# Kernel optimization log

Measured on AMD Instinct MI355X. Metric: run time of the kernel, lower is better.

Reference implementation:

```python
import jax, jax.numpy as jnp
import numpy as np

NEG_INF = -1e38


def wkv(k, v, w, u):
    """Log-sum-exp-stabilized RWKV WKV scan.
    k, v: (B, T, C); w, u: (C,). Returns y: (B, T, C).
    """
    B, T, C = k.shape

    def step(carry, kv_t):
        num, den, mx = carry            # each (B, C)
        k_t, v_t = kv_t                 # (B, C)
        ku = k_t + u
        m = jnp.maximum(mx, ku)
        e1 = jnp.exp(mx - m)
        e2 = jnp.exp(ku - m)
        y = (e1 * num + e2 * v_t) / (e1 * den + e2)
        # state update
        mw = mx + w
        m2 = jnp.maximum(mw, k_t)
        es1 = jnp.exp(mw - m2)
        es2 = jnp.exp(k_t - m2)
        num = es1 * num + es2 * v_t
        den = es1 * den + es2
        return (num, den, m2), y

    init = (jnp.zeros((B, C), k.dtype),
            jnp.zeros((B, C), k.dtype),
            jnp.full((B, C), NEG_INF, k.dtype))
    _, y = jax.lax.scan(step, init, (jnp.swapaxes(k, 0, 1), jnp.swapaxes(v, 0, 1)))
    return jnp.swapaxes(y, 0, 1)


def setup_inputs() -> dict:
    key = jax.random.key(0)
    ks = jax.random.split(key, 8)
    B, T, C = 8, 4096, 512
    x = jax.random.normal(ks[0], (B, T, C), dtype=jnp.float32)
    # Linear weights stored as (in, out) so forward is x @ W.
    W_rkv = jax.random.normal(ks[1], (C, 6 * C), dtype=jnp.float32) / np.sqrt(C)
    W_out = jax.random.normal(ks[2], (2 * C, C), dtype=jnp.float32) / np.sqrt(2 * C)
    time_decay = jax.random.uniform(ks[3], (C,), minval=-6.0, maxval=-5.0, dtype=jnp.float32)
    time_first = jax.random.uniform(ks[4], (C,), minval=-3.0, maxval=0.0, dtype=jnp.float32)
    time_decay_rev = jax.random.uniform(ks[5], (C,), minval=-6.0, maxval=-5.0, dtype=jnp.float32)
    time_first_rev = jax.random.uniform(ks[6], (C,), minval=-3.0, maxval=0.0, dtype=jnp.float32)
    return {"x": x, "W_rkv": W_rkv, "W_out": W_out,
            "time_decay": time_decay, "time_first": time_first,
            "time_decay_rev": time_decay_rev, "time_first_rev": time_first_rev}


def reference(x, W_rkv, W_out, time_decay, time_first, time_decay_rev, time_first_rev):
    B, T, C = x.shape
    rkv = (x @ W_rkv).reshape(B, T, 2, 3, C)
    # forward direction
    r_f, k_f, v_f = rkv[:, :, 0, 0], rkv[:, :, 0, 1], rkv[:, :, 0, 2]
    w_f = -jnp.exp(time_decay)
    out_f = jax.nn.sigmoid(r_f) * wkv(k_f, v_f, w_f, time_first)
    # backward direction (run scan on time-reversed k/v, then reverse back)
    r_b, k_b, v_b = rkv[:, :, 1, 0], rkv[:, :, 1, 1], rkv[:, :, 1, 2]
    w_b = -jnp.exp(time_decay_rev)
    out_b = wkv(k_b[:, ::-1], v_b[:, ::-1], w_b, time_first_rev)[:, ::-1]
    out_b = jax.nn.sigmoid(r_b) * out_b
    out_cat = jnp.concatenate([out_f, out_b], axis=-1)  # (B, T, 2C)
    return out_cat @ W_out
```

## Files before the change

### kernel.cpp

```cpp
#include <hip/hip_runtime.h>

typedef float f4 __attribute__((ext_vector_type(4)));
typedef unsigned short us4 __attribute__((ext_vector_type(4)));
typedef __bf16 bf16x8 __attribute__((ext_vector_type(8)));
typedef float f32x4 __attribute__((ext_vector_type(4)));
typedef _Float16 h4 __attribute__((ext_vector_type(4)));
typedef _Float16 h8 __attribute__((ext_vector_type(8)));

#define TT 4096
#define CCH 512
#define NCH2 256
#define CHL2 16
#define NSEG 32
#define SEGC 8

__device__ __forceinline__ unsigned short f2bf(float f) {
  unsigned u = __builtin_bit_cast(unsigned, f);
  unsigned r = (u + 0x7FFFu + ((u >> 16) & 1u)) >> 16;
  return (unsigned short)r;
}
__device__ __forceinline__ void gload_lds16(const void* g, void* l) {
  __builtin_amdgcn_global_load_lds(
      (const __attribute__((address_space(1))) unsigned int*)g,
      (__attribute__((address_space(3))) unsigned int*)l, 16, 0, 0);
}
#define VMCNT(n) asm volatile("s_waitcnt vmcnt(" #n ")" ::: "memory")

__global__ __launch_bounds__(256)
void convert_f32_bf16(const float* __restrict__ in, unsigned short* __restrict__ out, int n4) {
  int i = blockIdx.x * 256 + threadIdx.x;
  if (i >= n4) return;
  f4 f = *(const f4*)(in + (size_t)i * 4);
  us4 o = { f2bf(f[0]), f2bf(f[1]), f2bf(f[2]), f2bf(f[3]) };
  *(us4*)(out + (size_t)i * 4) = o;
}

__global__ __launch_bounds__(256)
void transpose_to_bf16(const float* __restrict__ in, unsigned short* __restrict__ out,
                       int R, int Cc) {
  __shared__ unsigned short tile[32][33];
  int c0 = blockIdx.x * 32, r0 = blockIdx.y * 32;
  int tx = threadIdx.x, ty = threadIdx.y;
  #pragma unroll
  for (int j = 0; j < 32; j += 8)
    tile[ty + j][tx] = f2bf(in[(size_t)(r0 + ty + j) * Cc + c0 + tx]);
  __syncthreads();
  #pragma unroll
  for (int j = 0; j < 32; j += 8)
    out[(size_t)(c0 + ty + j) * R + r0 + tx] = tile[tx][ty + j];
}

__global__ __launch_bounds__(512, 2)
void gemm256_g1(const unsigned short* __restrict__ A,
                const unsigned short* __restrict__ BT,
                _Float16* __restrict__ kbuf, _Float16* __restrict__ vbuf,
                _Float16* __restrict__ rbuf) {
  __shared__ char lds[131072];
  const int tid = threadIdx.x;
  const int lane = tid & 63, wv = tid >> 6;
  const int wm = wv >> 2, wn = wv & 3;
  const int ln15 = lane & 15, lq = lane >> 4;

  const int nwg = gridDim.x;
  const int bid = blockIdx.x;
  const int wgid = (nwg % 8 == 0) ? (bid % 8) * (nwg / 8) + bid / 8 : bid;
  const int bn = wgid % 12, bm = wgid / 12;
  const size_t m0 = (size_t)bm * 256, n0 = (size_t)bn * 256;
  const char* Ab = (const char*)(A + m0 * 512);
  const char* Bb = (const char*)(BT + n0 * 512);

  const int srow0 = tid >> 2, srow1 = 128 + (tid >> 2);
  const int sg = tid & 3;
  const int sgs0 = (sg ^ ((srow0 >> 1) & 3)) << 4;
  const int sgs1 = (sg ^ ((srow1 >> 1) & 3)) << 4;

  auto STAGE = [&](int mat, int t, int h) {
    const char* gsrc = mat ? Bb : Ab;
    char* ldst = lds + mat * 65536 + ((t & 1) << 15) + (h << 14);
    const size_t co = (size_t)t * 128 + (size_t)h * 64;
    gload_lds16(gsrc + (size_t)srow0 * 1024 + co + sgs0, ldst + tid * 16);
    gload_lds16(gsrc + (size_t)srow1 * 1024 + co + sgs1, ldst + 8192 + tid * 16);
  };

  f32x4 acc[8][4] = {};
  STAGE(0, 0, 0); STAGE(1, 0, 0); STAGE(0, 0, 1); STAGE(1, 0, 1);

  for (int t = 0; t < 8; ++t) {
    char* Abase = lds + ((t & 1) << 15);
    char* Bbase = lds + 65536 + ((t & 1) << 15);
    VMCNT(4);
    __builtin_amdgcn_s_barrier();
    __builtin_amdgcn_sched_barrier(0);
    {
      bf16x8 bf[4], af[8];
      #pragma unroll
      for (int fn = 0; fn < 4; ++fn) {
        const int r = wn * 64 + fn * 16 + ln15;
        bf[fn] = *(const bf16x8*)(Bbase + r * 64 + ((lq ^ ((r >> 1) & 3)) << 4));
      }
      #pragma unroll
      for (int fm = 0; fm < 8; ++fm) {
        const int r = wm * 128 + fm * 16 + ln15;
        af[fm] = *(const bf16x8*)(Abase + r * 64 + ((lq ^ ((r >> 1) & 3)) << 4));
      }
      if (t < 7) { STAGE(0, t + 1, 0); STAGE(1, t + 1, 0); }
      __builtin_amdgcn_s_setprio(1);
      #pragma unroll
      for (int fm = 0; fm < 8; ++fm)
        #pragma unroll
        for (int fn = 0; fn < 4; ++fn)
          acc[fm][fn] = __builtin_amdgcn_mfma_f32_16x16x32_bf16(af[fm], bf[fn], acc[fm][fn], 0, 0, 0);
      __builtin_amdgcn_s_setprio(0);
    }
    if (t < 7) { VMCNT(4); } else { VMCNT(0); }
    __builtin_amdgcn_s_barrier();
    __builtin_amdgcn_sched_barrier(0);
    {
      bf16x8 bf[4], af[8];
      #pragma unroll
      for (int fn = 0; fn < 4; ++fn) {
        const int r = wn * 64 + fn * 16 + ln15;
        bf[fn] = *(const bf16x8*)(Bbase + 16384 + r * 64 + ((lq ^ ((r >> 1) & 3)) << 4));
      }
      #pragma unroll
      for (int fm = 0; fm < 8; ++fm) {
        const int r = wm * 128 + fm * 16 + ln15;
        af[fm] = *(const bf16x8*)(Abase + 16384 + r * 64 + ((lq ^ ((r >> 1) & 3)) << 4));
      }
      if (t < 7) { STAGE(0, t + 1, 1); STAGE(1, t + 1, 1); }
      __builtin_amdgcn_s_setprio(1);
      #pragma unroll
      for (int fm = 0; fm < 8; ++fm)
        #pragma unroll
        for (int fn = 0; fn < 4; ++fn)
          acc[fm][fn] = __builtin_amdgcn_mfma_f32_16x16x32_bf16(af[fm], bf[fn], acc[fm][fn], 0, 0, 0);
      __builtin_amdgcn_s_setprio(0);
    }
  }

  const int n0i = (int)n0;
  const int dir = (n0i >= 1536) ? 1 : 0;
  const int jj0 = n0i - dir * 1536;
  const int seg = jj0 >> 9;
  const int cbase = jj0 & 511;
  _Float16* dbuf = (seg == 0) ? rbuf : (seg == 1 ? kbuf : vbuf);
  float* stg = (float*)lds;
  const int ebnd = wv >> 2;
  const int erow = (tid >> 3) & 31;
  const int el8 = tid & 7;
  __syncthreads();
  #pragma unroll
  for (int gi = 0; gi < 4; ++gi) {
    #pragma unroll
    for (int f2 = 0; f2 < 2; ++f2) {
      const int fm = gi * 2 + f2;
      #pragma unroll
      for (int q = 0; q < 4; ++q) {
        const int rloc = f2 * 16 + lq * 4 + q;
        float* dst = stg + wm * 8192 + rloc * 256;
        const int sw = ((rloc >> 2) & 1) << 4;
        #pragma unroll
        for (int fn = 0; fn < 4; ++fn)
          dst[(wn * 64 + fn * 16 + ln15) ^ sw] = acc[fm][fn][q];
      }
    }
    __syncthreads();
    {
      const int rowg = (int)m0 + ebnd * 128 + gi * 32 + erow;
      const int b_ = rowg >> 12, tt = rowg & 4095;
      const int trow = dir ? (4095 - tt) : tt;
      _Float16* gp = dbuf + ((size_t)(b_ * 2 + dir) * TT + trow) * 512 + cbase;
      const float* sp = stg + ebnd * 8192 + erow * 256;
      const int sw = ((erow >> 2) & 1) << 4;
      #pragma unroll
      for (int u = 0; u < 4; ++u) {
        const int cf = el8 * 8 + u * 64;
        const int cs = cf ^ sw;
        f4 a = *(const f4*)(sp + cs);
        f4 b = *(const f4*)(sp + cs + 4);
        h8 hv = { (_Float16)a[0], (_Float16)a[1], (_Float16)a[2], (_Float16)a[3],
                  (_Float16)b[0], (_Float16)b[1], (_Float16)b[2], (_Float16)b[3] };
        *(h8*)(gp + cf) = hv;
      }
    }
    __syncthreads();
  }
}

__global__ __launch_bounds__(256)
void gemm_bf16_m1(const unsigned short* __restrict__ A, int lda,
                  const unsigned short* __restrict__ BT, int ldb,
                  int M, int N, int K, float* __restrict__ out) {
  __shared__ char smem[16384];
  unsigned short* As  = (unsigned short*)smem;
  unsigned short* Bsm = (unsigned short*)(smem + 8192);
  const int tid = threadIdx.x;
  const int lane = tid & 63, wv = tid >> 6;
  const int wr = wv >> 1, wc = wv & 1;
  const int ln15 = lane & 15, lq = lane >> 4;
  const int mtiles = M >> 7;
  const int bm = blockIdx.x % mtiles, bn = blockIdx.x / mtiles;
  const size_t m0 = (size_t)bm << 7, n0 = (size_t)bn << 7;
  f32x4 acc[4][4] = {};
  const char* Ab = (const char*)(A + m0 * (size_t)lda);
  const char* Bb = (const char*)(BT + n0 * (size_t)ldb);
  const int r0 = tid >> 2;
  const int cb = (((tid & 3) ^ (r0 & 3)) << 4);
  const size_t ldab = (size_t)lda * 2, ldbb = (size_t)ldb * 2;

  for (int k0 = 0; k0 < K; k0 += 32) {
    const size_t kb = (size_t)k0 * 2;
    gload_lds16(Ab + (size_t)r0 * ldab + kb + cb,        (char*)As + tid * 16);
    gload_lds16(Ab + (size_t)(r0 + 64) * ldab + kb + cb, (char*)As + 4096 + tid * 16);
    gload_lds16(Bb + (size_t)r0 * ldbb + kb + cb,        (char*)Bsm + tid * 16);
    gload_lds16(Bb + (size_t)(r0 + 64) * ldbb + kb + cb, (char*)Bsm + 4096 + tid * 16);
    __syncthreads();
    bf16x8 af[4], bg[4];
    #pragma unroll
    for (int i = 0; i < 4; ++i) {
      const int ar = wr * 64 + i * 16 + ln15;
      const int br = wc * 64 + i * 16 + ln15;
      af[i] = *(const bf16x8*)((char*)As  + ((ar * 4 + (lq ^ (ar & 3))) << 4));
      bg[i] = *(const bf16x8*)((char*)Bsm + ((br * 4 + (lq ^ (br & 3))) << 4));
    }
    #pragma unroll
    for (int i = 0; i < 4; ++i)
      #pragma unroll
      for (int j = 0; j < 4; ++j)
        acc[i][j] = __builtin_amdgcn_mfma_f32_16x16x32_bf16(af[i], bg[j], acc[i][j], 0, 0, 0);
    __syncthreads();
  }

  const int tq = tid >> 3, t8 = tid & 7;
  #pragma unroll
  for (int i = 0; i < 4; ++i) {
    __syncthreads();
    float* st = (float*)smem;
    #pragma unroll
    for (int j = 0; j < 4; ++j) {
      const int cl = wc * 64 + j * 16 + ln15;
      #pragma unroll
      for (int q = 0; q < 4; ++q) {
        const int rl = wr * 16 + lq * 4 + q;
        st[rl * 128 + (cl ^ (((rl >> 2) & 3) << 4))] = acc[i][j][q];
      }
    }
    __syncthreads();
    const int rl = tq, lqp = (rl >> 2) & 3;
    const int lr = ((rl >> 4) << 6) + (i << 4) + (rl & 15);
    const int rowg = (int)m0 + lr;
    #pragma unroll
    for (int u = 0; u < 4; ++u) {
      const int colL = t8 * 16 + u * 4;
      const int colS = colL ^ (lqp << 4);
      f4 vv = *(const f4*)(st + rl * 128 + colS);
      *(f4*)(out + (size_t)rowg * N + n0 + colL) = vv;
    }
  }
}

__global__ __launch_bounds__(128)
void wkv_pass1(const _Float16* __restrict__ kbuf, const _Float16* __restrict__ vbuf,
               const float* __restrict__ td, const float* __restrict__ tdr,
               float* __restrict__ cN, float* __restrict__ cD, float* __restrict__ cM) {
  const int bd = blockIdx.x;
  const int ch = blockIdx.y;
  const int dir = bd & 1;
  const int c = threadIdx.x * 4;
  f4 tdv = *(const f4*)((dir ? tdr : td) + c);
  float w[4], num[4], den[4], m[4];
  #pragma unroll
  for (int e = 0; e < 4; ++e) { w[e] = -__expf(tdv[e]); num[e] = 0.f; den[e] = 0.f; m[e] = -1e38f; }
  const size_t base = ((size_t)bd * TT + (size_t)ch * CHL2) * CCH + c;
  const _Float16* kp = kbuf + base;
  const _Float16* vp = vbuf + base;
  h4 ka = *(const h4*)(kp), va = *(const h4*)(vp);
  h4 kb = *(const h4*)(kp + CCH), vb = *(const h4*)(vp + CCH);
  for (int t = 0; t < CHL2; ++t) {
    h4 kc = {}, vc = {};
    if (t + 2 < CHL2) {
      kc = *(const h4*)(kp + (size_t)(t + 2) * CCH);
      vc = *(const h4*)(vp + (size_t)(t + 2) * CCH);
    }
    #pragma unroll
    for (int e = 0; e < 4; ++e) {
      float ke = (float)ka[e], ve = (float)va[e];
      float mw = m[e] + w[e];
      float m2 = fmaxf(mw, ke);
      float e1 = __expf(mw - m2), e2 = __expf(ke - m2);
      num[e] = e1 * num[e] + e2 * ve;
      den[e] = e1 * den[e] + e2;
      m[e] = m2;
    }
    ka = kb; va = vb; kb = kc; vb = vc;
  }
  const size_t ci = ((size_t)bd * NCH2 + ch) * CCH + c;
  *(f4*)(cN + ci) = (f4){num[0], num[1], num[2], num[3]};
  *(f4*)(cD + ci) = (f4){den[0], den[1], den[2], den[3]};
  *(f4*)(cM + ci) = (f4){m[0], m[1], m[2], m[3]};
}

__global__ __launch_bounds__(128)
void wkv_p2a(const float* __restrict__ td, const float* __restrict__ tdr,
             const float* __restrict__ cN, const float* __restrict__ cD,
             const float* __restrict__ cM,
             float* __restrict__ scN, float* __restrict__ scD, float* __restrict__ scM) {
  const int bd = blockIdx.x, seg = blockIdx.y;
  const int dir = bd & 1;
  const int c = threadIdx.x * 4;
  f4 tdv = *(const f4*)((dir ? tdr : td) + c);
  float dw[4], num[4], den[4], m[4];
  #pragma unroll
  for (int e = 0; e < 4; ++e) { dw[e] = -__expf(tdv[e]) * (float)CHL2; num[e] = 0.f; den[e] = 0.f; m[e] = -1e38f; }
  size_t ci = ((size_t)bd * NCH2 + (size_t)seg * SEGC) * CCH + c;
  for (int j = 0; j < SEGC; ++j, ci += CCH) {
    f4 ln = *(const f4*)(cN + ci);
    f4 ld = *(const f4*)(cD + ci);
    f4 lm = *(const f4*)(cM + ci);
    #pragma unroll
    for (int e = 0; e < 4; ++e) {
      float mp = m[e] + dw[e];
      float mm = fmaxf(mp, lm[e]);
      float e1 = __expf(mp - mm), e2 = __expf(lm[e] - mm);
      num[e] = e1 * num[e] + e2 * ln[e];
      den[e] = e1 * den[e] + e2 * ld[e];
      m[e] = mm;
    }
  }
  const size_t si = ((size_t)bd * NSEG + seg) * CCH + c;
  *(f4*)(scN + si) = (f4){num[0], num[1], num[2], num[3]};
  *(f4*)(scD + si) = (f4){den[0], den[1], den[2], den[3]};
  *(f4*)(scM + si) = (f4){m[0], m[1], m[2], m[3]};
}

__global__ __launch_bounds__(128)
void wkv_p2b(const float* __restrict__ td, const float* __restrict__ tdr,
             float* __restrict__ scN, float* __restrict__ scD, float* __restrict__ scM) {
  const int bd = blockIdx.x;
  const int dir = bd & 1;
  const int c = threadIdx.x * 4;
  f4 tdv = *(const f4*)((dir ? tdr : td) + c);
  float dws[4], num[4], den[4], m[4];
  #pragma unroll
  for (int e = 0; e < 4; ++e) { dws[e] = -__expf(tdv[e]) * (float)(CHL2 * SEGC); num[e] = 0.f; den[e] = 0.f; m[e] = -1e38f; }
  size_t si = (size_t)bd * NSEG * CCH + c;
  for (int s = 0; s < NSEG; ++s, si += CCH) {
    f4 ln = *(const f4*)(scN + si);
    f4 ld = *(const f4*)(scD + si);
    f4 lm = *(const f4*)(scM + si);
    *(f4*)(scN + si) = (f4){num[0], num[1], num[2], num[3]};
    *(f4*)(scD + si) = (f4){den[0], den[1], den[2], den[3]};
    *(f4*)(scM + si) = (f4){m[0], m[1], m[2], m[3]};
    #pragma unroll
    for (int e = 0; e < 4; ++e) {
      float mp = m[e] + dws[e];
      float mm = fmaxf(mp, lm[e]);
      float e1 = __expf(mp - mm), e2 = __expf(lm[e] - mm);
      num[e] = e1 * num[e] + e2 * ln[e];
      den[e] = e1 * den[e] + e2 * ld[e];
      m[e] = mm;
    }
  }
}

__global__ __launch_bounds__(128)
void wkv_p2c(const float* __restrict__ td, const float* __restrict__ tdr,
             const float* __restrict__ scN, const float* __restrict__ scD,
             const float* __restrict__ scM,
             float* __restrict__ cN, float* __restrict__ cD, float* __restrict__ cM) {
  const int bd = blockIdx.x, seg = blockIdx.y;
  const int dir = bd & 1;
  const int c = threadIdx.x * 4;
  f4 tdv = *(const f4*)((dir ? tdr : td) + c);
  const size_t si = ((size_t)bd * NSEG + seg) * CCH + c;
  f4 nv = *(const f4*)(scN + si);
  f4 dv = *(const f4*)(scD + si);
  f4 mv = *(const f4*)(scM + si);
  float dw[4], num[4], den[4], m[4];
  #pragma unroll
  for (int e = 0; e < 4; ++e) {
    dw[e] = -__expf(tdv[e]) * (float)CHL2;
    num[e] = nv[e]; den[e] = dv[e]; m[e] = mv[e];
  }
  size_t ci = ((size_t)bd * NCH2 + (size_t)seg * SEGC) * CCH + c;
  for (int j = 0; j < SEGC; ++j, ci += CCH) {
    f4 ln = *(const f4*)(cN + ci);
    f4 ld = *(const f4*)(cD + ci);
    f4 lm = *(const f4*)(cM + ci);
    *(f4*)(cN + ci) = (f4){num[0], num[1], num[2], num[3]};
    *(f4*)(cD + ci) = (f4){den[0], den[1], den[2], den[3]};
    *(f4*)(cM + ci) = (f4){m[0], m[1], m[2], m[3]};
    #pragma unroll
    for (int e = 0; e < 4; ++e) {
      float mp = m[e] + dw[e];
      float mm = fmaxf(mp, lm[e]);
      float e1 = __expf(mp - mm), e2 = __expf(lm[e] - mm);
      num[e] = e1 * num[e] + e2 * ln[e];
      den[e] = e1 * den[e] + e2 * ld[e];
      m[e] = mm;
    }
  }
}

__global__ __launch_bounds__(128)
void wkv_pass3(const _Float16* __restrict__ kbuf, const _Float16* __restrict__ vbuf,
               const _Float16* __restrict__ rbuf,
               const float* __restrict__ td, const float* __restrict__ tf,
               const float* __restrict__ tdr, const float* __restrict__ tfr,
               const float* __restrict__ cN, const float* __restrict__ cD,
               const float* __restrict__ cM,
               unsigned short* __restrict__ ocat) {
  const int bd = blockIdx.x, ch = blockIdx.y;
  const int b = bd >> 1, dir = bd & 1;
  const int c = threadIdx.x * 4;
  f4 tdv = *(const f4*)((dir ? tdr : td) + c);
  f4 tuv = *(const f4*)((dir ? tfr : tf) + c);
  const size_t ci = ((size_t)bd * NCH2 + ch) * CCH + c;
  f4 nv = *(const f4*)(cN + ci);
  f4 dv = *(const f4*)(cD + ci);
  f4 mv = *(const f4*)(cM + ci);
  float w[4], u[4], num[4], den[4], m[4];
  #pragma unroll
  for (int e = 0; e < 4; ++e) {
    w[e] = -__expf(tdv[e]); u[e] = tuv[e];
    num[e] = nv[e]; den[e] = dv[e]; m[e] = mv[e];
  }
  const size_t base = ((size_t)bd * TT + (size_t)ch * CHL2) * CCH + c;
  const _Float16* kp = kbuf + base;
  const _Float16* vp = vbuf + base;
  const _Float16* rp = rbuf + base;
  h4 ka = *(const h4*)(kp), va = *(const h4*)(vp), ra = *(const h4*)(rp);
  h4 kb = *(const h4*)(kp + CCH), vb = *(const h4*)(vp + CCH), rb = *(const h4*)(rp + CCH);
  for (int t = 0; t < CHL2; ++t) {
    h4 kc = {}, vc = {}, rc = {};
    if (t + 2 < CHL2) {
      kc = *(const h4*)(kp + (size_t)(t + 2) * CCH);
      vc = *(const h4*)(vp + (size_t)(t + 2) * CCH);
      rc = *(const h4*)(rp + (size_t)(t + 2) * CCH);
    }
    const int tnat = ch * CHL2 + t;
    const int tact = dir ? (TT - 1 - tnat) : tnat;
    unsigned short o[4];
    #pragma unroll
    for (int e = 0; e < 4; ++e) {
      float ke = (float)ka[e], ve = (float)va[e];
      float ku = ke + u[e];
      float mm = fmaxf(m[e], ku);
      float e1 = __expf(m[e] - mm), e2 = __expf(ku - mm);
      float y = (e1 * num[e] + e2 * ve) * __builtin_amdgcn_rcpf(e1 * den[e] + e2);
      float rt = (float)ra[e];
      float sig = __builtin_amdgcn_rcpf(1.f + __expf(-rt));
      o[e] = f2bf(sig * y);
      float mw = m[e] + w[e];
      float m2 = fmaxf(mw, ke);
      float es1 = __expf(mw - m2), es2 = __expf(ke - m2);
      num[e] = es1 * num[e] + es2 * ve;
      den[e] = es1 * den[e] + es2;
      m[e] = m2;
    }
    *(us4*)(ocat + (((size_t)b * TT + tact) * 2 + dir) * CCH + c) = (us4){o[0], o[1], o[2], o[3]};
    ka = kb; va = vb; ra = rb; kb = kc; vb = vc; rb = rc;
  }
}

extern "C" void kernel_launch(void* const* d_in, const int* in_sizes, int n_in,
                              void* d_out, int out_size, void* d_ws, size_t ws_size,
                              hipStream_t stream) {
  const float* x   = (const float*)d_in[0];
  const float* Wr  = (const float*)d_in[1];
  const float* Wo  = (const float*)d_in[2];
  const float* td  = (const float*)d_in[3];
  const float* tf  = (const float*)d_in[4];
  const float* tdr = (const float*)d_in[5];
  const float* tfr = (const float*)d_in[6];
  float* out = (float*)d_out;

  auto rnd = [](size_t b) { return (b + 255) & ~(size_t)255; };
  const size_t wBytes = rnd((size_t)3072 * 512 * 2) + rnd((size_t)512 * 1024 * 2);
  auto need = [&](int Bs) {
    size_t s = wBytes;
    s += 3 * rnd((size_t)Bs * 2 * TT * 512 * 2);
    s += rnd((size_t)Bs * TT * 1024 * 2);
    s += 3 * rnd((size_t)Bs * 2 * (size_t)NCH2 * 512 * 4);
    s += 3 * rnd((size_t)Bs * 2 * (size_t)NSEG * 512 * 4);
    return s;
  };
  int Bs = 8;
  while (Bs > 1 && need(Bs) > ws_size) Bs >>= 1;

  char* ws = (char*)d_ws;
  size_t off = 0;
  auto alloc = [&](size_t bytes) -> char* {
    char* p = ws + off;
    off += (bytes + 255) & ~(size_t)255;
    return p;
  };
  unsigned short* wrkvT = (unsigned short*)alloc((size_t)3072 * 512 * 2);
  unsigned short* woutT = (unsigned short*)alloc((size_t)512 * 1024 * 2);
  _Float16*       kbuf  = (_Float16*)alloc((size_t)Bs * 2 * TT * 512 * 2);
  _Float16*       vbuf  = (_Float16*)alloc((size_t)Bs * 2 * TT * 512 * 2);
  _Float16*       rbuf  = (_Float16*)alloc((size_t)Bs * 2 * TT * 512 * 2);
  unsigned short* ocat  = (unsigned short*)alloc((size_t)Bs * TT * 1024 * 2);
  unsigned short* xb    = ocat;
  float*          cN    = (float*)alloc((size_t)Bs * 2 * (size_t)NCH2 * 512 * 4);
  float*          cD    = (float*)alloc((size_t)Bs * 2 * (size_t)NCH2 * 512 * 4);
  float*          cM    = (float*)alloc((size_t)Bs * 2 * (size_t)NCH2 * 512 * 4);
  float*          scN   = (float*)alloc((size_t)Bs * 2 * (size_t)NSEG * 512 * 4);
  float*          scD   = (float*)alloc((size_t)Bs * 2 * (size_t)NSEG * 512 * 4);
  float*          scM   = (float*)alloc((size_t)Bs * 2 * (size_t)NSEG * 512 * 4);

  transpose_to_bf16<<<dim3(3072 / 32, 512 / 32), dim3(32, 8), 0, stream>>>(Wr, wrkvT, 512, 3072);
  transpose_to_bf16<<<dim3(512 / 32, 1024 / 32), dim3(32, 8), 0, stream>>>(Wo, woutT, 1024, 512);

  const int nslices = 8 / Bs;
  const int Mslice = Bs * TT;
  const int mt256 = Mslice >> 8;
  const int mt128 = Mslice >> 7;
  for (int s = 0; s < nslices; ++s) {
    const float* xs = x + (size_t)s * Mslice * 512;
    float* outs = out + (size_t)s * Mslice * 512;
    convert_f32_bf16<<<Mslice * 512 / 1024, 256, 0, stream>>>(xs, xb, Mslice * 512 / 4);
    gemm256_g1<<<mt256 * 12, 512, 0, stream>>>(xb, wrkvT, kbuf, vbuf, rbuf);
    wkv_pass1<<<dim3(Bs * 2, NCH2), 128, 0, stream>>>(kbuf, vbuf, td, tdr, cN, cD, cM);
    wkv_p2a<<<dim3(Bs * 2, NSEG), 128, 0, stream>>>(td, tdr, cN, cD, cM, scN, scD, scM);
    wkv_p2b<<<Bs * 2, 128, 0, stream>>>(td, tdr, scN, scD, scM);
    wkv_p2c<<<dim3(Bs * 2, NSEG), 128, 0, stream>>>(td, tdr, scN, scD, scM, cN, cD, cM);
    wkv_pass3<<<dim3(Bs * 2, NCH2), 128, 0, stream>>>(kbuf, vbuf, rbuf, td, tf, tdr, tfr,
                                                      cN, cD, cM, ocat);
    gemm_bf16_m1<<<mt128 * 4, 256, 0, stream>>>(ocat, 1024, woutT, 1024, Mslice, 512, 1024, outs);
  }
}
```

Before: 371.0 us.

## Split GEMM k-loop into four phases interleaving LDS reads, staging and MFMA

Restructures the projection GEMM main loop into four sub-phases per k-tile, each loading half the A fragments (B fragments reused across two phases), issuing one matrix's next-tile global-to-LDS stage, then running 16 MFMAs. Barriers and explicit lgkmcnt/vmcnt waits are placed per phase to interleave memory traffic with compute and cut register pressure. It adds more barriers per iteration, which may cost synchronization overhead.

Result: no change. 374.0 us (+0.8%).

```diff
diff --git a/kernel.cpp b/kernel.cpp
--- a/kernel.cpp
+++ b/kernel.cpp
@@ -25,6 +25,7 @@
       (__attribute__((address_space(3))) unsigned int*)l, 16, 0, 0);
 }
 #define VMCNT(n) asm volatile("s_waitcnt vmcnt(" #n ")" ::: "memory")
+#define LGKMCNT0 asm volatile("s_waitcnt lgkmcnt(0)" ::: "memory")
 
 __global__ __launch_bounds__(256)
 void convert_f32_bf16(const float* __restrict__ in, unsigned short* __restrict__ out, int n4) {
@@ -83,58 +84,47 @@
   };
 
   f32x4 acc[8][4] = {};
+  bf16x8 bfr[4];
+
   STAGE(0, 0, 0); STAGE(1, 0, 0); STAGE(0, 0, 1); STAGE(1, 0, 1);
-
-  for (int t = 0; t < 8; ++t) {
-    char* Abase = lds + ((t & 1) << 15);
-    char* Bbase = lds + 65536 + ((t & 1) << 15);
-    VMCNT(4);
-    __builtin_amdgcn_s_barrier();
-    __builtin_amdgcn_sched_barrier(0);
-    {
-      bf16x8 bf[4], af[8];
+  VMCNT(4);
+  __builtin_amdgcn_s_barrier();
+
+  for (int kt = 0; kt < 8; ++kt) {
+    const char* Abase = lds + ((kt & 1) << 15);
+    const char* Bbase = lds + 65536 + ((kt & 1) << 15);
+    #pragma unroll
+    for (int p = 0; p < 4; ++p) {
+      const int ks = p >> 1;
+      const int fmb = (p & 1) << 2;
+      const int hb = ks << 14;
+      if ((p & 1) == 0) {
+        #pragma unroll
+        for (int fn = 0; fn < 4; ++fn) {
+          const int r = wn * 64 + fn * 16 + ln15;
+          bfr[fn] = *(const bf16x8*)(Bbase + hb + r * 64 + ((lq ^ ((r >> 1) & 3)) << 4));
+        }
+      }
+      bf16x8 af[4];
       #pragma unroll
-      for (int fn = 0; fn < 4; ++fn) {
-        const int r = wn * 64 + fn * 16 + ln15;
-        bf[fn] = *(const bf16x8*)(Bbase + r * 64 + ((lq ^ ((r >> 1) & 3)) << 4));
+      for (int i = 0; i < 4; ++i) {
+        const int r = wm * 128 + (fmb + i) * 16 + ln15;
+        af[i] = *(const bf16x8*)(Abase + hb + r * 64 + ((lq ^ ((r >> 1) & 3)) << 4));
       }
-      #pragma unroll
-      for (int fm = 0; fm < 8; ++fm) {
-        const int r = wm * 128 + fm * 16 + ln15;
-        af[fm] = *(const bf16x8*)(Abase + r * 64 + ((lq ^ ((r >> 1) & 3)) << 4));
-      }
-      if (t < 7) { STAGE(0, t + 1, 0); STAGE(1, t + 1, 0); }
+      if (kt < 7) STAGE(p & 1, kt + 1, ks);
+      __builtin_amdgcn_s_barrier();
+      LGKMCNT0;
+      __builtin_amdgcn_sched_barrier(0);
       __builtin_amdgcn_s_setprio(1);
       #pragma unroll
-      for (int fm = 0; fm < 8; ++fm)
+      for (int i = 0; i < 4; ++i)
         #pragma unroll
         for (int fn = 0; fn < 4; ++fn)
-          acc[fm][fn] = __builtin_amdgcn_mfma_f32_16x16x32_bf16(af[fm], bf[fn], acc[fm][fn], 0, 0, 0);
+          acc[fmb + i][fn] = __builtin_amdgcn_mfma_f32_16x16x32_bf16(af[i], bfr[fn], acc[fmb + i][fn], 0, 0, 0);
       __builtin_amdgcn_s_setprio(0);
-    }
-    if (t < 7) { VMCNT(4); } else { VMCNT(0); }
-    __builtin_amdgcn_s_barrier();
-    __builtin_amdgcn_sched_barrier(0);
-    {
-      bf16x8 bf[4], af[8];
-      #pragma unroll
-      for (int fn = 0; fn < 4; ++fn) {
-        const int r = wn * 64 + fn * 16 + ln15;
-        bf[fn] = *(const bf16x8*)(Bbase + 16384 + r * 64 + ((lq ^ ((r >> 1) & 3)) << 4));
-      }
-      #pragma unroll
-      for (int fm = 0; fm < 8; ++fm) {
-        const int r = wm * 128 + fm * 16 + ln15;
-        af[fm] = *(const bf16x8*)(Abase + 16384 + r * 64 + ((lq ^ ((r >> 1) & 3)) << 4));
-      }
-      if (t < 7) { STAGE(0, t + 1, 1); STAGE(1, t + 1, 1); }
-      __builtin_amdgcn_s_setprio(1);
-      #pragma unroll
-      for (int fm = 0; fm < 8; ++fm)
-        #pragma unroll
-        for (int fn = 0; fn < 4; ++fn)
-          acc[fm][fn] = __builtin_amdgcn_mfma_f32_16x16x32_bf16(af[fm], bf[fn], acc[fm][fn], 0, 0, 0);
-      __builtin_amdgcn_s_setprio(0);
+      if (p == 1) { if (kt < 7) { VMCNT(4); } else { VMCNT(0); } }
+      else if (p == 3) { if (kt < 7) { VMCNT(4); } }
+      __builtin_amdgcn_s_barrier();
     }
   }
 
```
